# Kernel tuning notes

Measured on AMD Instinct MI355X. Metric: run time of the kernel, lower is better.

The kernel has to match this reference:

```python
import jax, jax.numpy as jnp
import numpy as np
from jax import lax

N, D, H, E = 8192, 1024, 4096, 8


def setup_inputs() -> dict:
    key = jax.random.key(0)
    ks = jax.random.split(key, 7)
    s = 0.02
    return {
        "x": jax.random.normal(ks[0], (N, D), dtype=jnp.float32),
        "Wr": jax.random.normal(ks[1], (E, D), dtype=jnp.float32) * s,
        "br": jnp.zeros((E,), dtype=jnp.float32),
        "Wup": jax.random.normal(ks[2], (E, H, D), dtype=jnp.float32) * s,
        "bup": jnp.zeros((E, H), dtype=jnp.float32),
        "Wdown": jax.random.normal(ks[3], (E, D, H), dtype=jnp.float32) * s,
        "bdown": jnp.zeros((E, D), dtype=jnp.float32),
    }


def reference(x, Wr, br, Wup, bup, Wdown, bdown):
    # Router: softmax over logits; only argmax is used (softmax is monotone,
    # argmax of softmax == argmax of logits).
    logits = x @ Wr.T + br            # [N, E]
    scores = jax.nn.softmax(logits, axis=-1)
    top1 = jnp.argmax(scores, axis=-1)  # [N] int

    out0 = jnp.zeros_like(x)

    def body(out, ew):
        i, Wu, bu, Wd, bd = ew
        h = jax.nn.silu(x @ Wu.T + bu)   # [N, H]
        y = h @ Wd.T + bd                # [N, D]
        out = jnp.where((top1 == i)[:, None], y, out)
        return out, None

    idx = jnp.arange(Wup.shape[0])
    out, _ = lax.scan(body, out0, (idx, Wup, bup, Wdown, bdown))
    return out
```

## Files before the change

kernel.cpp:

```cpp
#include <hip/hip_runtime.h>

#define NT 8192
#define DD 1024
#define HH 4096
#define EE 8

typedef __attribute__((ext_vector_type(8))) short short8;
typedef __attribute__((ext_vector_type(4))) float f32x4;

__device__ __forceinline__ unsigned short f2bf(float f) {
    unsigned int u = __float_as_uint(f);
    u += 0x7FFFu + ((u >> 16) & 1u);
    return (unsigned short)(u >> 16);
}

__device__ __forceinline__ void gload_lds16(const void* g, void* l) {
    __builtin_amdgcn_global_load_lds(
        (const __attribute__((address_space(1))) unsigned int*)g,
        (__attribute__((address_space(3))) unsigned int*)l, 16, 0, 0);
}

__global__ __launch_bounds__(256) void cvtw_kernel(const float* __restrict__ a,
                                                   const float* __restrict__ b,
                                                   unsigned short* __restrict__ da,
                                                   unsigned short* __restrict__ db) {
    const size_t half = (size_t)EE * HH * DD;
    size_t i = ((size_t)blockIdx.x * 256 + threadIdx.x) * 4;
    const float* s; unsigned short* d;
    if (i < half) { s = a + i; d = da + i; }
    else          { s = b + (i - half); d = db + (i - half); }
    float4 v = *(const float4*)s;
    ushort4 o;
    o.x = f2bf(v.x); o.y = f2bf(v.y); o.z = f2bf(v.z); o.w = f2bf(v.w);
    *(ushort4*)d = o;
}

__global__ __launch_bounds__(256) void router_kernel(const float* __restrict__ x,
                                                     const float* __restrict__ Wr,
                                                     const float* __restrict__ br,
                                                     int* __restrict__ counts,
                                                     int* __restrict__ tlist) {
    __shared__ float sW[EE * DD];
    const int t = threadIdx.x;
    for (int i = t; i < EE * DD / 4; i += 256)
        ((float4*)sW)[i] = ((const float4*)Wr)[i];
    __syncthreads();
    const int lane = t & 63;
    const int wv = t >> 6;
    const int token = blockIdx.x * 4 + wv;
    const float* xr = x + (size_t)token * DD;
    float acc[EE];
#pragma unroll
    for (int e = 0; e < EE; e++) acc[e] = 0.f;
    for (int k = lane; k < DD; k += 64) {
        float xv = xr[k];
#pragma unroll
        for (int e = 0; e < EE; e++) acc[e] += xv * sW[e * DD + k];
    }
#pragma unroll
    for (int off = 32; off > 0; off >>= 1) {
#pragma unroll
        for (int e = 0; e < EE; e++) acc[e] += __shfl_xor(acc[e], off);
    }
    if (lane == 0) {
        int best = 0;
        float bv = acc[0] + br[0];
#pragma unroll
        for (int e = 1; e < EE; e++) {
            float v = acc[e] + br[e];
            if (v > bv) { bv = v; best = e; }
        }
        int pos = atomicAdd(&counts[best], 1);
        tlist[best * NT + pos] = token;
    }
}

__global__ __launch_bounds__(256) void gather_kernel(const float* __restrict__ x,
                                                     const int* __restrict__ tlist,
                                                     const int* __restrict__ counts,
                                                     unsigned short* __restrict__ xg) {
    const int row = blockIdx.x * 4 + (threadIdx.x >> 6);
    const int lane = threadIdx.x & 63;
    int off[EE];
    int s = 0;
#pragma unroll
    for (int k = 0; k < EE; k++) { off[k] = s; s += counts[k]; }
    int e = 0;
#pragma unroll
    for (int k = 1; k < EE; k++)
        if (row >= off[k]) e = k;
    const int token = tlist[e * NT + row - off[e]];
    const float4* src = (const float4*)(x + (size_t)token * DD);
    ushort4* dst = (ushort4*)(xg + (size_t)row * DD);
#pragma unroll
    for (int it = 0; it < 4; it++) {
        float4 v = src[it * 64 + lane];
        ushort4 o;
        o.x = f2bf(v.x); o.y = f2bf(v.y); o.z = f2bf(v.z); o.w = f2bf(v.w);
        dst[it * 64 + lane] = o;
    }
}


__global__ __launch_bounds__(256) void up_gemm(const unsigned short* __restrict__ xg,
                                               const unsigned short* __restrict__ Wub,
                                               const float* __restrict__ bup,
                                               const int* __restrict__ counts,
                                               unsigned short* __restrict__ hbuf) {
    const int e = blockIdx.z;
    int off_e = 0, cnt;
    {
        int s = 0;
#pragma unroll
        for (int k = 0; k < EE; k++) { if (k == e) off_e = s; s += counts[k]; }
        cnt = counts[e];
    }
    const int m0 = blockIdx.y * 128;
    if (m0 >= cnt) return;
    const int n0 = blockIdx.x * 128;
    const int t = threadIdx.x;

    __shared__ unsigned short sA[128 * 32];
    __shared__ unsigned short sB[128 * 32];

    const int r0 = t >> 2;
    const int kc = (t & 3) ^ ((r0 >> 1) & 3);
    const int c1 = cnt - 1;
    int ra = m0 + r0;      if (ra > c1) ra = c1;
    int rb = m0 + 64 + r0; if (rb > c1) rb = c1;
    const unsigned short* gA0 = xg + (size_t)(off_e + ra) * DD + kc * 8;
    const unsigned short* gA1 = xg + (size_t)(off_e + rb) * DD + kc * 8;
    const unsigned short* gB0 = Wub + ((size_t)e * HH + n0 + r0) * DD + kc * 8;
    const unsigned short* gB1 = Wub + ((size_t)e * HH + n0 + 64 + r0) * DD + kc * 8;
    unsigned short* lA0 = sA + t * 8;
    unsigned short* lA1 = sA + (t + 256) * 8;
    unsigned short* lB0 = sB + t * 8;
    unsigned short* lB1 = sB + (t + 256) * 8;

    const int lane = t & 63;
    const int wm = ((t >> 6) & 1) * 64;
    const int wn = (t >> 7) * 64;
    const int mrow = lane & 15;
    const int kq = lane >> 4;
    const int slot = (kq ^ ((mrow >> 1) & 3)) * 8;

    f32x4 acc[4][4];
#pragma unroll
    for (int i = 0; i < 4; i++)
#pragma unroll
        for (int j = 0; j < 4; j++)
            acc[i][j] = (f32x4){0.f, 0.f, 0.f, 0.f};

    for (int kt = 0; kt < DD; kt += 32) {
        __syncthreads();
        gload_lds16(gA0 + kt, lA0);
        gload_lds16(gA1 + kt, lA1);
        gload_lds16(gB0 + kt, lB0);
        gload_lds16(gB1 + kt, lB1);
        __syncthreads();
        short8 a[4], b[4];
#pragma unroll
        for (int i = 0; i < 4; i++) {
            a[i] = *(const short8*)(sA + (wm + i * 16 + mrow) * 32 + slot);
            b[i] = *(const short8*)(sB + (wn + i * 16 + mrow) * 32 + slot);
        }
#pragma unroll
        for (int i = 0; i < 4; i++)
#pragma unroll
            for (int j = 0; j < 4; j++)
                acc[i][j] = __builtin_amdgcn_mfma_f32_16x16x32_bf16(a[i], b[j], acc[i][j], 0, 0, 0);
    }

    float bias[4];
#pragma unroll
    for (int j = 0; j < 4; j++) bias[j] = bup[e * HH + n0 + wn + j * 16 + mrow];
#pragma unroll
    for (int i = 0; i < 4; i++) {
#pragma unroll
        for (int r = 0; r < 4; r++) {
            int m = m0 + wm + i * 16 + kq * 4 + r;
            if (m < cnt) {
                unsigned short* hrow = hbuf + (size_t)(off_e + m) * HH + n0 + wn + mrow;
#pragma unroll
                for (int j = 0; j < 4; j++) {
                    float v = acc[i][j][r] + bias[j];
                    v = v / (1.f + __expf(-v));
                    hrow[j * 16] = f2bf(v);
                }
            }
        }
    }
}

__global__ __launch_bounds__(256) void down_gemm(const unsigned short* __restrict__ hbuf,
                                                 const unsigned short* __restrict__ Wdb,
                                                 const float* __restrict__ bdown,
                                                 const int* __restrict__ counts,
                                                 const int* __restrict__ tlist,
                                                 float* __restrict__ out) {
    const int e = blockIdx.z;
    int off_e = 0, cnt;
    {
        int s = 0;
#pragma unroll
        for (int k = 0; k < EE; k++) { if (k == e) off_e = s; s += counts[k]; }
        cnt = counts[e];
    }
    const int m0 = blockIdx.y * 128;
    if (m0 >= cnt) return;
    const int n0 = blockIdx.x * 128;
    const int t = threadIdx.x;

    __shared__ unsigned short sA[128 * 32];
    __shared__ unsigned short sB[128 * 32];

    const int r0 = t >> 2;
    const int kc = (t & 3) ^ ((r0 >> 1) & 3);
    const int c1 = cnt - 1;
    int ra = m0 + r0;      if (ra > c1) ra = c1;
    int rb = m0 + 64 + r0; if (rb > c1) rb = c1;
    const unsigned short* gA0 = hbuf + (size_t)(off_e + ra) * HH + kc * 8;
    const unsigned short* gA1 = hbuf + (size_t)(off_e + rb) * HH + kc * 8;
    const unsigned short* gB0 = Wdb + ((size_t)e * DD + n0 + r0) * HH + kc * 8;
    const unsigned short* gB1 = Wdb + ((size_t)e * DD + n0 + 64 + r0) * HH + kc * 8;
    unsigned short* lA0 = sA + t * 8;
    unsigned short* lA1 = sA + (t + 256) * 8;
    unsigned short* lB0 = sB + t * 8;
    unsigned short* lB1 = sB + (t + 256) * 8;

    const int lane = t & 63;
    const int wm = ((t >> 6) & 1) * 64;
    const int wn = (t >> 7) * 64;
    const int mrow = lane & 15;
    const int kq = lane >> 4;
    const int slot = (kq ^ ((mrow >> 1) & 3)) * 8;

    f32x4 acc[4][4];
#pragma unroll
    for (int i = 0; i < 4; i++)
#pragma unroll
        for (int j = 0; j < 4; j++)
            acc[i][j] = (f32x4){0.f, 0.f, 0.f, 0.f};

    for (int kt = 0; kt < HH; kt += 32) {
        __syncthreads();
        gload_lds16(gA0 + kt, lA0);
        gload_lds16(gA1 + kt, lA1);
        gload_lds16(gB0 + kt, lB0);
        gload_lds16(gB1 + kt, lB1);
        __syncthreads();
        short8 a[4], b[4];
#pragma unroll
        for (int i = 0; i < 4; i++) {
            a[i] = *(const short8*)(sA + (wm + i * 16 + mrow) * 32 + slot);
            b[i] = *(const short8*)(sB + (wn + i * 16 + mrow) * 32 + slot);
        }
#pragma unroll
        for (int i = 0; i < 4; i++)
#pragma unroll
            for (int j = 0; j < 4; j++)
                acc[i][j] = __builtin_amdgcn_mfma_f32_16x16x32_bf16(a[i], b[j], acc[i][j], 0, 0, 0);
    }

    const int* tl = tlist + e * NT;
    float bias[4];
#pragma unroll
    for (int j = 0; j < 4; j++) bias[j] = bdown[e * DD + n0 + wn + j * 16 + mrow];
#pragma unroll
    for (int i = 0; i < 4; i++) {
#pragma unroll
        for (int r = 0; r < 4; r++) {
            int m = m0 + wm + i * 16 + kq * 4 + r;
            if (m < cnt) {
                int token = tl[m];
                float* orow = out + (size_t)token * DD + n0 + wn + mrow;
#pragma unroll
                for (int j = 0; j < 4; j++)
                    orow[j * 16] = acc[i][j][r] + bias[j];
            }
        }
    }
}

extern "C" void kernel_launch(void* const* d_in, const int* in_sizes, int n_in,
                              void* d_out, int out_size, void* d_ws, size_t ws_size,
                              hipStream_t stream) {
    const float* x     = (const float*)d_in[0];
    const float* Wr    = (const float*)d_in[1];
    const float* br    = (const float*)d_in[2];
    const float* Wup   = (const float*)d_in[3];
    const float* bup   = (const float*)d_in[4];
    const float* Wdown = (const float*)d_in[5];
    const float* bdown = (const float*)d_in[6];
    float* out = (float*)d_out;

    char* w = (char*)d_ws;
    int* counts  = (int*)w;               w += 256;
    int* tlist   = (int*)w;               w += (size_t)EE * NT * 4;
    unsigned short* xg   = (unsigned short*)w;  w += (size_t)NT * DD * 2;
    unsigned short* hbuf = (unsigned short*)w;  w += (size_t)NT * HH * 2;
    unsigned short* Wub  = (unsigned short*)w;  w += (size_t)EE * HH * DD * 2;
    unsigned short* Wdb  = (unsigned short*)w;

    hipMemsetAsync(counts, 0, EE * sizeof(int), stream);

    cvtw_kernel<<<(2 * (size_t)EE * HH * DD) / 1024, 256, 0, stream>>>(Wup, Wdown, Wub, Wdb);
    router_kernel<<<NT / 4, 256, 0, stream>>>(x, Wr, br, counts, tlist);
    gather_kernel<<<NT / 4, 256, 0, stream>>>(x, tlist, counts, xg);

    dim3 gu(HH / 128, NT / 128, EE);
    up_gemm<<<gu, 256, 0, stream>>>(xg, Wub, bup, counts, hbuf);
    dim3 gd(DD / 128, NT / 128, EE);
    down_gemm<<<gd, 256, 0, stream>>>(hbuf, Wdb, bdown, counts, tlist, out);
}
```

Measured before the change: 660.9 us.

## Double-buffer LDS tiles in expert GEMMs and widen down-GEMM K tile

Both expert GEMMs now keep two LDS stages and prefetch the next K tile while computing the current one, using a single barrier per iteration. The down GEMM also doubles its K tile to 64 with an 8-way XOR swizzle, halving the number of barriers over the long K loop. The weight-conversion kernel handles eight elements per thread. The costs are doubled LDS use, which may lower occupancy, and overlap that is limited because the barrier waits on all outstanding loads.

```diff
diff --git a/kernel.cpp b/kernel.cpp
--- a/kernel.cpp
+++ b/kernel.cpp
@@ -25,14 +25,17 @@
                                                    unsigned short* __restrict__ da,
                                                    unsigned short* __restrict__ db) {
     const size_t half = (size_t)EE * HH * DD;
-    size_t i = ((size_t)blockIdx.x * 256 + threadIdx.x) * 4;
+    size_t i = ((size_t)blockIdx.x * 256 + threadIdx.x) * 8;
     const float* s; unsigned short* d;
     if (i < half) { s = a + i; d = da + i; }
     else          { s = b + (i - half); d = db + (i - half); }
-    float4 v = *(const float4*)s;
-    ushort4 o;
-    o.x = f2bf(v.x); o.y = f2bf(v.y); o.z = f2bf(v.z); o.w = f2bf(v.w);
-    *(ushort4*)d = o;
+    float4 v0 = ((const float4*)s)[0];
+    float4 v1 = ((const float4*)s)[1];
+    ushort4 o0, o1;
+    o0.x = f2bf(v0.x); o0.y = f2bf(v0.y); o0.z = f2bf(v0.z); o0.w = f2bf(v0.w);
+    o1.x = f2bf(v1.x); o1.y = f2bf(v1.y); o1.z = f2bf(v1.z); o1.w = f2bf(v1.w);
+    ((ushort4*)d)[0] = o0;
+    ((ushort4*)d)[1] = o1;
 }
 
 __global__ __launch_bounds__(256) void router_kernel(const float* __restrict__ x,
@@ -120,8 +123,8 @@
     const int n0 = blockIdx.x * 128;
     const int t = threadIdx.x;
 
-    __shared__ unsigned short sA[128 * 32];
-    __shared__ unsigned short sB[128 * 32];
+    __shared__ unsigned short sA[2][128 * 32];
+    __shared__ unsigned short sB[2][128 * 32];
 
     const int r0 = t >> 2;
     const int kc = (t & 3) ^ ((r0 >> 1) & 3);
@@ -132,10 +135,6 @@
     const unsigned short* gA1 = xg + (size_t)(off_e + rb) * DD + kc * 8;
     const unsigned short* gB0 = Wub + ((size_t)e * HH + n0 + r0) * DD + kc * 8;
     const unsigned short* gB1 = Wub + ((size_t)e * HH + n0 + 64 + r0) * DD + kc * 8;
-    unsigned short* lA0 = sA + t * 8;
-    unsigned short* lA1 = sA + (t + 256) * 8;
-    unsigned short* lB0 = sB + t * 8;
-    unsigned short* lB1 = sB + (t + 256) * 8;
 
     const int lane = t & 63;
     const int wm = ((t >> 6) & 1) * 64;
@@ -151,24 +150,30 @@
         for (int j = 0; j < 4; j++)
             acc[i][j] = (f32x4){0.f, 0.f, 0.f, 0.f};
 
+    auto STAGE = [&](int buf, int kt) {
+        gload_lds16(gA0 + kt, &sA[buf][t * 8]);
+        gload_lds16(gA1 + kt, &sA[buf][(t + 256) * 8]);
+        gload_lds16(gB0 + kt, &sB[buf][t * 8]);
+        gload_lds16(gB1 + kt, &sB[buf][(t + 256) * 8]);
+    };
+
+    STAGE(0, 0);
+    int cur = 0;
     for (int kt = 0; kt < DD; kt += 32) {
         __syncthreads();
-        gload_lds16(gA0 + kt, lA0);
-        gload_lds16(gA1 + kt, lA1);
-        gload_lds16(gB0 + kt, lB0);
-        gload_lds16(gB1 + kt, lB1);
-        __syncthreads();
+        if (kt + 32 < DD) STAGE(cur ^ 1, kt + 32);
         short8 a[4], b[4];
 #pragma unroll
         for (int i = 0; i < 4; i++) {
-            a[i] = *(const short8*)(sA + (wm + i * 16 + mrow) * 32 + slot);
-            b[i] = *(const short8*)(sB + (wn + i * 16 + mrow) * 32 + slot);
+            a[i] = *(const short8*)(&sA[cur][(wm + i * 16 + mrow) * 32 + slot]);
+            b[i] = *(const short8*)(&sB[cur][(wn + i * 16 + mrow) * 32 + slot]);
         }
 #pragma unroll
         for (int i = 0; i < 4; i++)
 #pragma unroll
             for (int j = 0; j < 4; j++)
                 acc[i][j] = __builtin_amdgcn_mfma_f32_16x16x32_bf16(a[i], b[j], acc[i][j], 0, 0, 0);
+        cur ^= 1;
     }
 
     float bias[4];
@@ -211,29 +216,28 @@
     const int n0 = blockIdx.x * 128;
     const int t = threadIdx.x;
 
-    __shared__ unsigned short sA[128 * 32];
-    __shared__ unsigned short sB[128 * 32];
-
-    const int r0 = t >> 2;
-    const int kc = (t & 3) ^ ((r0 >> 1) & 3);
+    __shared__ unsigned short sA[2][128 * 64];
+    __shared__ unsigned short sB[2][128 * 64];
+
+    const int r = t >> 3;
+    const int c = t & 7;
     const int c1 = cnt - 1;
-    int ra = m0 + r0;      if (ra > c1) ra = c1;
-    int rb = m0 + 64 + r0; if (rb > c1) rb = c1;
-    const unsigned short* gA0 = hbuf + (size_t)(off_e + ra) * HH + kc * 8;
-    const unsigned short* gA1 = hbuf + (size_t)(off_e + rb) * HH + kc * 8;
-    const unsigned short* gB0 = Wdb + ((size_t)e * DD + n0 + r0) * HH + kc * 8;
-    const unsigned short* gB1 = Wdb + ((size_t)e * DD + n0 + 64 + r0) * HH + kc * 8;
-    unsigned short* lA0 = sA + t * 8;
-    unsigned short* lA1 = sA + (t + 256) * 8;
-    unsigned short* lB0 = sB + t * 8;
-    unsigned short* lB1 = sB + (t + 256) * 8;
+    const unsigned short* gA[4];
+    const unsigned short* gB[4];
+#pragma unroll
+    for (int i = 0; i < 4; i++) {
+        int row = r + 32 * i;
+        int sc = c ^ (row & 7);
+        int ra = m0 + row; if (ra > c1) ra = c1;
+        gA[i] = hbuf + (size_t)(off_e + ra) * HH + sc * 8;
+        gB[i] = Wdb + ((size_t)e * DD + n0 + row) * HH + sc * 8;
+    }
 
     const int lane = t & 63;
     const int wm = ((t >> 6) & 1) * 64;
     const int wn = (t >> 7) * 64;
     const int mrow = lane & 15;
     const int kq = lane >> 4;
-    const int slot = (kq ^ ((mrow >> 1) & 3)) * 8;
 
     f32x4 acc[4][4];
 #pragma unroll
@@ -242,24 +246,36 @@
         for (int j = 0; j < 4; j++)
             acc[i][j] = (f32x4){0.f, 0.f, 0.f, 0.f};
 
-    for (int kt = 0; kt < HH; kt += 32) {
+    auto STAGE = [&](int buf, int kt) {
+#pragma unroll
+        for (int i = 0; i < 4; i++)
+            gload_lds16(gA[i] + kt, &sA[buf][(i * 256 + t) * 8]);
+#pragma unroll
+        for (int i = 0; i < 4; i++)
+            gload_lds16(gB[i] + kt, &sB[buf][(i * 256 + t) * 8]);
+    };
+
+    STAGE(0, 0);
+    int cur = 0;
+    for (int kt = 0; kt < HH; kt += 64) {
         __syncthreads();
-        gload_lds16(gA0 + kt, lA0);
-        gload_lds16(gA1 + kt, lA1);
-        gload_lds16(gB0 + kt, lB0);
-        gload_lds16(gB1 + kt, lB1);
-        __syncthreads();
-        short8 a[4], b[4];
-#pragma unroll
-        for (int i = 0; i < 4; i++) {
-            a[i] = *(const short8*)(sA + (wm + i * 16 + mrow) * 32 + slot);
-            b[i] = *(const short8*)(sB + (wn + i * 16 + mrow) * 32 + slot);
-        }
-#pragma unroll
-        for (int i = 0; i < 4; i++)
-#pragma unroll
-            for (int j = 0; j < 4; j++)
-                acc[i][j] = __builtin_amdgcn_mfma_f32_16x16x32_bf16(a[i], b[j], acc[i][j], 0, 0, 0);
+        if (kt + 64 < HH) STAGE(cur ^ 1, kt + 64);
+#pragma unroll
+        for (int h = 0; h < 2; h++) {
+            const int slot = (((h << 2) | kq) ^ (mrow & 7)) * 8;
+            short8 a[4], b[4];
+#pragma unroll
+            for (int i = 0; i < 4; i++) {
+                a[i] = *(const short8*)(&sA[cur][(wm + i * 16 + mrow) * 64 + slot]);
+                b[i] = *(const short8*)(&sB[cur][(wn + i * 16 + mrow) * 64 + slot]);
+            }
+#pragma unroll
+            for (int i = 0; i < 4; i++)
+#pragma unroll
+                for (int j = 0; j < 4; j++)
+                    acc[i][j] = __builtin_amdgcn_mfma_f32_16x16x32_bf16(a[i], b[j], acc[i][j], 0, 0, 0);
+        }
+        cur ^= 1;
     }
 
     const int* tl = tlist + e * NT;
@@ -269,14 +285,14 @@
 #pragma unroll
     for (int i = 0; i < 4; i++) {
 #pragma unroll
-        for (int r = 0; r < 4; r++) {
-            int m = m0 + wm + i * 16 + kq * 4 + r;
+        for (int r2 = 0; r2 < 4; r2++) {
+            int m = m0 + wm + i * 16 + kq * 4 + r2;
             if (m < cnt) {
                 int token = tl[m];
                 float* orow = out + (size_t)token * DD + n0 + wn + mrow;
 #pragma unroll
                 for (int j = 0; j < 4; j++)
-                    orow[j * 16] = acc[i][j][r] + bias[j];
+                    orow[j * 16] = acc[i][j][r2] + bias[j];
             }
         }
     }
@@ -304,7 +320,7 @@
 
     hipMemsetAsync(counts, 0, EE * sizeof(int), stream);
 
-    cvtw_kernel<<<(2 * (size_t)EE * HH * DD) / 1024, 256, 0, stream>>>(Wup, Wdown, Wub, Wdb);
+    cvtw_kernel<<<(2 * (size_t)EE * HH * DD) / 2048, 256, 0, stream>>>(Wup, Wdown, Wub, Wdb);
     router_kernel<<<NT / 4, 256, 0, stream>>>(x, Wr, br, counts, tlist);
     gather_kernel<<<NT / 4, 256, 0, stream>>>(x, tlist, counts, xg);
 
```

Result: slower. 724.3 us (+9.6%).
